# Kernel tuning notes

Measured on AMD Instinct MI355X. Metric: run time of the kernel, lower is better.

The kernel has to match this reference:

```python
import jax, jax.numpy as jnp
import numpy as np

B, N, D, H = 4, 2048, 256, 8
DH = D // H  # 32
EPS = 1e-5


def layernorm(x, g, b):
    mu = jnp.mean(x, axis=-1, keepdims=True)
    var = jnp.mean(jnp.square(x - mu), axis=-1, keepdims=True)
    return (x - mu) * jax.lax.rsqrt(var + EPS) * g + b


def setup_inputs() -> dict:
    key = jax.random.key(0)
    ks = jax.random.split(key, 16)
    s = 1.0 / np.sqrt(D)
    p = lambda k: jax.random.uniform(k, (D, D), jnp.float32, -s, s)
    return {
        "qdt": jax.random.normal(ks[0], (B, N, D), jnp.float32),
        "boxes": jax.random.normal(ks[1], (B, N, D), jnp.float32),
        "mask": jax.random.randint(ks[2], (N, N), 0, 2, jnp.int32),
        "Wq": p(ks[3]), "bq": jnp.zeros((D,), jnp.float32),
        "Wk": p(ks[4]), "bk": jnp.zeros((D,), jnp.float32),
        "Wv": p(ks[5]), "bv": jnp.zeros((D,), jnp.float32),
        "Wo": p(ks[6]), "bo": jnp.zeros((D,), jnp.float32),
        "W1": p(ks[7]), "b1": jnp.zeros((D,), jnp.float32),
        "W2": p(ks[8]), "b2": jnp.zeros((D,), jnp.float32),
        "g1": jnp.ones((D,), jnp.float32), "be1": jnp.zeros((D,), jnp.float32),
        "g2": jnp.ones((D,), jnp.float32), "be2": jnp.zeros((D,), jnp.float32),
    }


def reference(qdt, boxes, mask, Wq, bq, Wk, bk, Wv, bv, Wo, bo,
              W1, b1, W2, b2, g1, be1, g2, be2):
    # q = k = tgt = boxes + qdt  (dropout in eval mode -> identity)
    x = boxes + qdt  # [B,N,D]
    q = (x @ Wq + bq).reshape(B, N, H, DH)
    k = (x @ Wk + bk).reshape(B, N, H, DH)
    v = (x @ Wv + bv).reshape(B, N, H, DH)
    scores = jnp.einsum('bqhd,bkhd->bhqk', q, k) / np.sqrt(DH)
    # masked_fill(mask==0, -inf) then sigmoid  ==  sigmoid gated to 0 where masked
    attn = jnp.where(mask.astype(bool)[None, None, :, :],
                     jax.nn.sigmoid(scores), 0.0)
    o = jnp.einsum('bhqk,bkhd->bqhd', attn, v).reshape(B, N, D)
    attn_out = o @ Wo + bo
    tgt = layernorm(x + attn_out, g1, be1)
    ff = jax.nn.relu(tgt @ W1 + b1) @ W2 + b2
    tgt = layernorm(tgt + ff, g2, be2)
    return tgt
```

## Files before the change

### kernel.cpp

```cpp
#include <hip/hip_runtime.h>
#include <hip/hip_bf16.h>

typedef unsigned short u16;
typedef unsigned int u32;
typedef __attribute__((ext_vector_type(8))) short bf16x8;
typedef __attribute__((ext_vector_type(4))) float f32x4;

#define BB 4
#define NN 2048
#define DD 256
#define HH 8
#define LAMBDA (-0.2550351f)

__device__ inline u16 bfu(float f) {
  __hip_bfloat16 h = __float2bfloat16(f);
  return *reinterpret_cast<u16*>(&h);
}
__device__ inline bf16x8 asfrag(uint4 v) { return __builtin_bit_cast(bf16x8, v); }

__global__ __launch_bounds__(256) void prep_kernel(
    const float* __restrict__ qdt, const float* __restrict__ boxes,
    const int* __restrict__ mask,
    const float* __restrict__ Wq, const float* __restrict__ Wk, const float* __restrict__ Wv,
    const float* __restrict__ Wo, const float* __restrict__ W1, const float* __restrict__ W2,
    const float* __restrict__ bq, const float* __restrict__ bk, const float* __restrict__ bv,
    float* __restrict__ xp, u16* __restrict__ xb, unsigned char* __restrict__ m8,
    u16* __restrict__ wqkvT, u16* __restrict__ woT, u16* __restrict__ w1T, u16* __restrict__ w2T,
    float* __restrict__ bqkv) {
  const int bid = blockIdx.x, t = threadIdx.x;
  if (bid < 2048) {
    int i = bid * 256 + t;
    int row = i >> 6, q = i & 63;
    float4 a = ((const float4*)qdt)[i];
    float4 b = ((const float4*)boxes)[i];
    float4 v = make_float4(a.x + b.x, a.y + b.y, a.z + b.z, a.w + b.w);
    ((ushort4*)xb)[i] = make_ushort4(bfu(v.x), bfu(v.y), bfu(v.z), bfu(v.w));
    float* xr = xp + (size_t)row * 256;
    xr[((4*q+0) & 15) * 16 + ((4*q+0) >> 4)] = v.x;
    xr[((4*q+1) & 15) * 16 + ((4*q+1) >> 4)] = v.y;
    xr[((4*q+2) & 15) * 16 + ((4*q+2) >> 4)] = v.z;
    xr[((4*q+3) & 15) * 16 + ((4*q+3) >> 4)] = v.w;
  } else if (bid < 6144) {
    int i = (bid - 2048) * 256 + t;
    int4 m = ((const int4*)mask)[i];
    ((uchar4*)m8)[i] = make_uchar4((unsigned char)m.x, (unsigned char)m.y,
                                   (unsigned char)m.z, (unsigned char)m.w);
  } else {
    int i = (bid - 6144) * 256 + t;
    if (i < 196608) {
      int n = i >> 8, k = i & 255;
      const float* src = (n < 256) ? Wq : (n < 512 ? Wk : Wv);
      wqkvT[i] = bfu(src[k * 256 + (n & 255)]);
    } else if (i < 262144) {
      int j = i - 196608; int n = j >> 8, k = j & 255;
      woT[j] = bfu(Wo[k * 256 + n]);
    } else if (i < 327680) {
      int j = i - 262144; int n = j >> 8, k = j & 255;
      w1T[j] = bfu(W1[k * 256 + n]);
    } else if (i < 393216) {
      int j = i - 327680; int n = j >> 8, k = j & 255;
      w2T[j] = bfu(W2[k * 256 + n]);
    } else if (i < 393984) {
      int n = i - 393216;
      bqkv[n] = (n < 256) ? bq[n] : (n < 512 ? bk[n - 256] : bv[n - 512]);
    }
  }
}

__global__ __launch_bounds__(256) void gemm_qkvt_kernel(
    const u16* __restrict__ xb, const u16* __restrict__ wqkvT,
    const float* __restrict__ bqkv,
    u16* __restrict__ qout, u16* __restrict__ kout, u16* __restrict__ vtout) {
  __shared__ u16 At[64][264];
  __shared__ u16 Bs[64][264];
  const int bid = blockIdx.x;
  const bool isqk = bid < 1024;
  const u16* A  = isqk ? xb : (wqkvT + 512 * 256);
  const u16* Bt = isqk ? wqkvT : xb;
  const int m0 = isqk ? (bid >> 3) * 64 : ((bid - 1024) >> 7) * 64;
  const int n0 = isqk ? (bid & 7) * 64 : ((bid - 1024) & 127) * 64;
  const int t = threadIdx.x;
  {
    const int row = t >> 2, cb = (t & 3) * 64;
    const u16* ga = A  + (size_t)(m0 + row) * 256 + cb;
    const u16* gb = Bt + (size_t)(n0 + row) * 256 + cb;
#pragma unroll
    for (int i = 0; i < 8; ++i) {
      *(int4*)&At[row][cb + i * 8] = *(const int4*)(ga + i * 8);
      *(int4*)&Bs[row][cb + i * 8] = *(const int4*)(gb + i * 8);
    }
  }
  __syncthreads();
  const int w = t >> 6, l = t & 63, g = l >> 4, c = l & 15;
  f32x4 acc[4] = {};
#pragma unroll
  for (int kk = 0; kk < 256; kk += 32) {
    bf16x8 af = *(const bf16x8*)&At[w * 16 + c][kk + g * 8];
#pragma unroll
    for (int j = 0; j < 4; ++j) {
      bf16x8 bfr = *(const bf16x8*)&Bs[j * 16 + c][kk + g * 8];
      acc[j] = __builtin_amdgcn_mfma_f32_16x16x32_bf16(af, bfr, acc[j], 0, 0, 0);
    }
  }
  if (isqk) {
    if (n0 < 256) {
#pragma unroll
      for (int j = 0; j < 4; ++j)
#pragma unroll
        for (int r = 0; r < 4; ++r) {
          int m = m0 + w * 16 + g * 4 + r, n = n0 + j * 16 + c;
          qout[(size_t)m * 256 + n] = bfu((acc[j][r] + bqkv[n]) * LAMBDA);
        }
    } else {
#pragma unroll
      for (int j = 0; j < 4; ++j)
#pragma unroll
        for (int r = 0; r < 4; ++r) {
          int m = m0 + w * 16 + g * 4 + r, n = n0 + j * 16 + c;
          int ch = n - 256;
          kout[(size_t)((m >> 11) * 8 + (ch >> 5)) * 65536 + (size_t)(m & 2047) * 32 + (ch & 31)]
              = bfu(acc[j][r] + bqkv[n]);
        }
    }
  } else {
#pragma unroll
    for (int j = 0; j < 4; ++j)
#pragma unroll
      for (int r = 0; r < 4; ++r) {
        int m = m0 + w * 16 + g * 4 + r;
        int n = n0 + j * 16 + c;
        vtout[(size_t)m * 8192 + n] = bfu(acc[j][r] + bqkv[512 + m]);
      }
  }
}

__global__ __launch_bounds__(256) void attn_kernel(
    const u16* __restrict__ qb,
    const u16* __restrict__ kb,
    const u16* __restrict__ vtb,
    const unsigned char* __restrict__ m8,
    u16* __restrict__ ob) {
  __shared__ u32 Klds[2][64][20];
  __shared__ u32 Vlds[2][32][36];
  __shared__ unsigned char Mlds[2][64][64];
  __shared__ u32 Plds[4][16][36];

  const int bid = blockIdx.x;
  const int qt = bid & 31, h = (bid >> 5) & 7, b = bid >> 8;
  const int q0 = qt * 64;
  const int t = threadIdx.x, w = t >> 6, l = t & 63, g = l >> 4, c = l & 15;

  const bf16x8 qf = asfrag(*(const uint4*)(qb + (size_t)(b * NN + q0 + 16 * w + c) * 256 + h * 32 + 8 * g));
  f32x4 oacc[2] = {};

  const int srowK = t >> 2, ssegK = t & 3;
  const int srowV = t >> 3, ssegV = t & 7;
  const u16* kg = kb + (size_t)(b * 8 + h) * 65536 + srowK * 32 + ssegK * 8;
  const u16* vg = vtb + (size_t)(h * 32 + srowV) * 8192 + (size_t)b * NN + ssegV * 8;
  const unsigned char* mg = m8 + (size_t)(q0 + srowK) * NN + ssegK * 16;

  const int mb0 = (16 * ssegK + 8 * (srowK & 7)) & 63;
  const int mb1 = (mb0 + 8) & 63;

  uint4 krg = *(const uint4*)kg;
  uint4 vrg = *(const uint4*)vg;
  uint4 mrg = *(const uint4*)mg;
  *(uint4*)&Klds[0][srowK][ssegK * 4] = krg;
  *(uint4*)&Vlds[0][srowV][ssegV * 4] = vrg;
  *(uint2*)&Mlds[0][srowK][mb0] = make_uint2(mrg.x, mrg.y);
  *(uint2*)&Mlds[0][srowK][mb1] = make_uint2(mrg.z, mrg.w);
  __syncthreads();

  const f32x4 zf = {0.f, 0.f, 0.f, 0.f};
  u32* Pw = &Plds[w][0][0];

  for (int it = 0; it < 32; ++it) {
    const int cur = it & 1;
    if (it < 31) {
      const int kt = (it + 1) * 64;
      krg = *(const uint4*)(kg + (size_t)kt * 32);
      vrg = *(const uint4*)(vg + kt);
      mrg = *(const uint4*)(mg + kt);
    }
#pragma unroll
    for (int tt = 0; tt < 4; ++tt) {
      bf16x8 kf = asfrag(*(const uint4*)&Klds[cur][16 * tt + c][4 * g]);
      f32x4 s = __builtin_amdgcn_mfma_f32_16x16x32_bf16(kf, qf, zf, 0, 0, 0);
      u32 mdw = *(const u32*)&Mlds[cur][16 * w + c][(16 * tt + 4 * g + 8 * (c & 7)) & 63];
      float mf0 = (float)(mdw & 0xffu);
      float mf1 = (float)((mdw >> 8) & 0xffu);
      float mf2 = (float)((mdw >> 16) & 0xffu);
      float mf3 = (float)(mdw >> 24);
      float p0 = mf0 * __builtin_amdgcn_rcpf(1.f + __builtin_amdgcn_exp2f(s[0]));
      float p1 = mf1 * __builtin_amdgcn_rcpf(1.f + __builtin_amdgcn_exp2f(s[1]));
      float p2 = mf2 * __builtin_amdgcn_rcpf(1.f + __builtin_amdgcn_exp2f(s[2]));
      float p3 = mf3 * __builtin_amdgcn_rcpf(1.f + __builtin_amdgcn_exp2f(s[3]));
      u32 w0, w1;
      asm("v_cvt_pk_bf16_f32 %0, %1, %2" : "=v"(w0) : "v"(p0), "v"(p1));
      asm("v_cvt_pk_bf16_f32 %0, %1, %2" : "=v"(w1) : "v"(p2), "v"(p3));
      *(uint2*)&Pw[c * 36 + 8 * tt + 2 * g] = make_uint2(w0, w1);
    }
    asm volatile("s_waitcnt lgkmcnt(0)" ::: "memory");
    __builtin_amdgcn_sched_barrier(0);
#pragma unroll
    for (int kk = 0; kk < 2; ++kk) {
      bf16x8 pf = asfrag(*(const uint4*)&Pw[c * 36 + 16 * kk + 4 * g]);
#pragma unroll
      for (int d0 = 0; d0 < 2; ++d0) {
        bf16x8 vf = asfrag(*(const uint4*)&Vlds[cur][16 * d0 + c][16 * kk + 4 * g]);
        oacc[d0] = __builtin_amdgcn_mfma_f32_16x16x32_bf16(pf, vf, oacc[d0], 0, 0, 0);
      }
    }
    if (it < 31) {
      *(uint4*)&Klds[cur ^ 1][srowK][ssegK * 4] = krg;
      *(uint4*)&Vlds[cur ^ 1][srowV][ssegV * 4] = vrg;
      *(uint2*)&Mlds[cur ^ 1][srowK][mb0] = make_uint2(mrg.x, mrg.y);
      *(uint2*)&Mlds[cur ^ 1][srowK][mb1] = make_uint2(mrg.z, mrg.w);
    }
    __syncthreads();
  }

  const size_t obase = (size_t)(b * NN + q0 + 16 * w) * 256 + h * 32;
#pragma unroll
  for (int d0 = 0; d0 < 2; ++d0)
#pragma unroll
    for (int r = 0; r < 4; ++r)
      ob[obase + (size_t)(4 * g + r) * 256 + 16 * d0 + c] = bfu(oacc[d0][r]);
}

__global__ __launch_bounds__(256) void tail_kernel(
    const u16* __restrict__ obuf, const u16* __restrict__ woT,
    const u16* __restrict__ w1T, const u16* __restrict__ w2T,
    const float* __restrict__ xp,
    const float* __restrict__ bo, const float* __restrict__ b1, const float* __restrict__ b2,
    const float* __restrict__ g1, const float* __restrict__ be1,
    const float* __restrict__ g2, const float* __restrict__ be2,
    float* __restrict__ out) {
  __shared__ u16 A[16][264];
  __shared__ float T1[16][260];
  __shared__ float PS1[16][4], PS2[16][4];
  const int t = threadIdx.x, w = t >> 6, l = t & 63, g = l >> 4, c = l & 15;
  const int m0 = blockIdx.x * 16;
  const int n0 = w * 64;
  const f32x4 zf4 = {0.f, 0.f, 0.f, 0.f};

  {
    const int srow = t >> 4, sseg = t & 15;
#pragma unroll
    for (int i = 0; i < 2; ++i) {
      uint4 v = *(const uint4*)(obuf + (size_t)(m0 + srow) * 256 + (sseg + 16 * i) * 8);
      *(uint4*)&A[srow][(sseg + 16 * i) * 8] = v;
    }
  }
  __syncthreads();

  f32x4 acc[4];
  float mean[4], inv[4];

#pragma unroll
  for (int j = 0; j < 4; ++j) acc[j] = zf4;
#pragma unroll
  for (int kk = 0; kk < 256; kk += 32) {
    bf16x8 af = *(const bf16x8*)&A[c][kk + 8 * g];
#pragma unroll
    for (int j = 0; j < 4; ++j) {
      bf16x8 bfr = asfrag(*(const uint4*)(woT + (size_t)(n0 + 16 * j + c) * 256 + kk + 8 * g));
      acc[j] = __builtin_amdgcn_mfma_f32_16x16x32_bf16(af, bfr, acc[j], 0, 0, 0);
    }
  }
  {
    float bov[4];
#pragma unroll
    for (int j = 0; j < 4; ++j) bov[j] = bo[n0 + 16 * j + c];
#pragma unroll
    for (int r = 0; r < 4; ++r) {
      float4 xq = ((const float4*)(xp + (size_t)(m0 + 4 * g + r) * 256 + c * 16))[w];
      float xa[4] = {xq.x, xq.y, xq.z, xq.w};
      float a1 = 0.f, a2 = 0.f;
#pragma unroll
      for (int j = 0; j < 4; ++j) {
        float z = acc[j][r] + bov[j] + xa[j];
        T1[4 * g + r][n0 + 16 * j + c] = z;
        a1 += z; a2 += z * z;
      }
#pragma unroll
      for (int off = 1; off < 16; off <<= 1) {
        a1 += __shfl_xor(a1, off);
        a2 += __shfl_xor(a2, off);
      }
      if (c == 0) { PS1[4 * g + r][w] = a1; PS2[4 * g + r][w] = a2; }
    }
  }
  __syncthreads();
#pragma unroll
  for (int r = 0; r < 4; ++r) {
    const int row = 4 * g + r;
    float s1 = PS1[row][0] + PS1[row][1] + PS1[row][2] + PS1[row][3];
    float s2 = PS2[row][0] + PS2[row][1] + PS2[row][2] + PS2[row][3];
    mean[r] = s1 * (1.f / 256.f);
    inv[r] = rsqrtf(s2 * (1.f / 256.f) - mean[r] * mean[r] + 1e-5f);
  }
#pragma unroll
  for (int j = 0; j < 4; ++j) {
    const int n = n0 + 16 * j + c;
    const float gv = g1[n], bev = be1[n];
#pragma unroll
    for (int r = 0; r < 4; ++r) {
      float v = (T1[4 * g + r][n] - mean[r]) * inv[r] * gv + bev;
      T1[4 * g + r][n] = v;
      A[4 * g + r][n] = bfu(v);
    }
  }
  __syncthreads();

#pragma unroll
  for (int j = 0; j < 4; ++j) acc[j] = zf4;
#pragma unroll
  for (int kk = 0; kk < 256; kk += 32) {
    bf16x8 af = *(const bf16x8*)&A[c][kk + 8 * g];
#pragma unroll
    for (int j = 0; j < 4; ++j) {
      bf16x8 bfr = asfrag(*(const uint4*)(w1T + (size_t)(n0 + 16 * j + c) * 256 + kk + 8 * g));
      acc[j] = __builtin_amdgcn_mfma_f32_16x16x32_bf16(af, bfr, acc[j], 0, 0, 0);
    }
  }
  __syncthreads();
#pragma unroll
  for (int j = 0; j < 4; ++j) {
    const int n = n0 + 16 * j + c;
    const float bv = b1[n];
#pragma unroll
    for (int r = 0; r < 4; ++r) {
      float v = acc[j][r] + bv;
      A[4 * g + r][n] = bfu(v > 0.f ? v : 0.f);
    }
  }
  __syncthreads();

#pragma unroll
  for (int j = 0; j < 4; ++j) acc[j] = zf4;
#pragma unroll
  for (int kk = 0; kk < 256; kk += 32) {
    bf16x8 af = *(const bf16x8*)&A[c][kk + 8 * g];
#pragma unroll
    for (int j = 0; j < 4; ++j) {
      bf16x8 bfr = asfrag(*(const uint4*)(w2T + (size_t)(n0 + 16 * j + c) * 256 + kk + 8 * g));
      acc[j] = __builtin_amdgcn_mfma_f32_16x16x32_bf16(af, bfr, acc[j], 0, 0, 0);
    }
  }
  {
    float b2v[4];
#pragma unroll
    for (int j = 0; j < 4; ++j) b2v[j] = b2[n0 + 16 * j + c];
#pragma unroll
    for (int r = 0; r < 4; ++r) {
      float a1 = 0.f, a2 = 0.f;
#pragma unroll
      for (int j = 0; j < 4; ++j) {
        const int n = n0 + 16 * j + c;
        float z = acc[j][r] + b2v[j] + T1[4 * g + r][n];
        T1[4 * g + r][n] = z;
        a1 += z; a2 += z * z;
      }
#pragma unroll
      for (int off = 1; off < 16; off <<= 1) {
        a1 += __shfl_xor(a1, off);
        a2 += __shfl_xor(a2, off);
      }
      if (c == 0) { PS1[4 * g + r][w] = a1; PS2[4 * g + r][w] = a2; }
    }
  }
  __syncthreads();
#pragma unroll
  for (int r = 0; r < 4; ++r) {
    const int row = 4 * g + r;
    float s1 = PS1[row][0] + PS1[row][1] + PS1[row][2] + PS1[row][3];
    float s2 = PS2[row][0] + PS2[row][1] + PS2[row][2] + PS2[row][3];
    mean[r] = s1 * (1.f / 256.f);
    inv[r] = rsqrtf(s2 * (1.f / 256.f) - mean[r] * mean[r] + 1e-5f);
  }
#pragma unroll
  for (int j = 0; j < 4; ++j) {
    const int n = n0 + 16 * j + c;
    const float gv = g2[n], bev = be2[n];
#pragma unroll
    for (int r = 0; r < 4; ++r)
      out[(size_t)(m0 + 4 * g + r) * 256 + n] = (T1[4 * g + r][n] - mean[r]) * inv[r] * gv + bev;
  }
}

extern "C" void kernel_launch(void* const* d_in, const int* in_sizes, int n_in,
                              void* d_out, int out_size, void* d_ws, size_t ws_size,
                              hipStream_t stream) {
  const float* qdt   = (const float*)d_in[0];
  const float* boxes = (const float*)d_in[1];
  const int*   mask  = (const int*)d_in[2];
  const float* Wq = (const float*)d_in[3];
  const float* bq = (const float*)d_in[4];
  const float* Wk = (const float*)d_in[5];
  const float* bk = (const float*)d_in[6];
  const float* Wv = (const float*)d_in[7];
  const float* bv = (const float*)d_in[8];
  const float* Wo = (const float*)d_in[9];
  const float* bo = (const float*)d_in[10];
  const float* W1 = (const float*)d_in[11];
  const float* b1 = (const float*)d_in[12];
  const float* W2 = (const float*)d_in[13];
  const float* b2 = (const float*)d_in[14];
  const float* g1  = (const float*)d_in[15];
  const float* be1 = (const float*)d_in[16];
  const float* g2  = (const float*)d_in[17];
  const float* be2 = (const float*)d_in[18];

  char* ws = (char*)d_ws;
  float* xp    = (float*)(ws + 0);
  u16*   xb    = (u16*)  (ws + 8388608);
  u16*   qbuf  = (u16*)  (ws + 12582912);
  u16*   kbuf  = (u16*)  (ws + 16777216);
  u16*   vtbuf = (u16*)  (ws + 20971520);
  u16*   obuf  = (u16*)  (ws + 25165824);
  u16*   wqkvT = (u16*)  (ws + 46137344);
  u16*   woT   = (u16*)  (ws + 46530560);
  u16*   w1T   = (u16*)  (ws + 46661632);
  u16*   w2T   = (u16*)  (ws + 46792704);
  float* bqkv  = (float*)(ws + 46923776);
  unsigned char* m8 = (unsigned char*)(ws + 46926848);

  prep_kernel<<<7683, 256, 0, stream>>>(qdt, boxes, mask, Wq, Wk, Wv, Wo, W1, W2,
                                        bq, bk, bv, xp, xb, m8,
                                        wqkvT, woT, w1T, w2T, bqkv);
  gemm_qkvt_kernel<<<1536, 256, 0, stream>>>(xb, wqkvT, bqkv, qbuf, kbuf, vtbuf);
  attn_kernel<<<1024, 256, 0, stream>>>(qbuf, kbuf, vtbuf, m8, obuf);
  tail_kernel<<<512, 256, 0, stream>>>(obuf, woT, w1T, w2T, xp,
                                       bo, b1, b2, g1, be1, g2, be2, (float*)d_out);
}
```

Before: 112.9 us.

## Process 32 rows per tail block and keep residual in registers

```diff
diff --git a/kernel.cpp b/kernel.cpp
--- a/kernel.cpp
+++ b/kernel.cpp
@@ -236,36 +236,39 @@
     const float* __restrict__ g1, const float* __restrict__ be1,
     const float* __restrict__ g2, const float* __restrict__ be2,
     float* __restrict__ out) {
-  __shared__ u16 A[16][264];
-  __shared__ float T1[16][260];
-  __shared__ float PS1[16][4], PS2[16][4];
+  __shared__ u16 A[32][264];
+  __shared__ float PS1[32][4], PS2[32][4];
   const int t = threadIdx.x, w = t >> 6, l = t & 63, g = l >> 4, c = l & 15;
-  const int m0 = blockIdx.x * 16;
+  const int m0 = blockIdx.x * 32;
   const int n0 = w * 64;
   const f32x4 zf4 = {0.f, 0.f, 0.f, 0.f};
 
   {
-    const int srow = t >> 4, sseg = t & 15;
-#pragma unroll
-    for (int i = 0; i < 2; ++i) {
-      uint4 v = *(const uint4*)(obuf + (size_t)(m0 + srow) * 256 + (sseg + 16 * i) * 8);
-      *(uint4*)&A[srow][(sseg + 16 * i) * 8] = v;
-    }
-  }
-  __syncthreads();
-
-  f32x4 acc[4];
-  float mean[4], inv[4];
-
-#pragma unroll
-  for (int j = 0; j < 4; ++j) acc[j] = zf4;
+    const int srow = t >> 3, sseg = t & 7;
+#pragma unroll
+    for (int i = 0; i < 4; ++i) {
+      uint4 v = *(const uint4*)(obuf + (size_t)(m0 + srow) * 256 + (sseg + 8 * i) * 8);
+      *(uint4*)&A[srow][(sseg + 8 * i) * 8] = v;
+    }
+  }
+  __syncthreads();
+
+  f32x4 acc[2][4], t1[2][4];
+  float mean[2][4], inv[2][4];
+
+#pragma unroll
+  for (int rg = 0; rg < 2; ++rg)
+#pragma unroll
+    for (int j = 0; j < 4; ++j) acc[rg][j] = zf4;
 #pragma unroll
   for (int kk = 0; kk < 256; kk += 32) {
-    bf16x8 af = *(const bf16x8*)&A[c][kk + 8 * g];
+    bf16x8 af0 = *(const bf16x8*)&A[c][kk + 8 * g];
+    bf16x8 af1 = *(const bf16x8*)&A[16 + c][kk + 8 * g];
 #pragma unroll
     for (int j = 0; j < 4; ++j) {
       bf16x8 bfr = asfrag(*(const uint4*)(woT + (size_t)(n0 + 16 * j + c) * 256 + kk + 8 * g));
-      acc[j] = __builtin_amdgcn_mfma_f32_16x16x32_bf16(af, bfr, acc[j], 0, 0, 0);
+      acc[0][j] = __builtin_amdgcn_mfma_f32_16x16x32_bf16(af0, bfr, acc[0][j], 0, 0, 0);
+      acc[1][j] = __builtin_amdgcn_mfma_f32_16x16x32_bf16(af1, bfr, acc[1][j], 0, 0, 0);
     }
   }
   {
@@ -273,55 +276,66 @@
 #pragma unroll
     for (int j = 0; j < 4; ++j) bov[j] = bo[n0 + 16 * j + c];
 #pragma unroll
+    for (int rg = 0; rg < 2; ++rg)
+#pragma unroll
+      for (int r = 0; r < 4; ++r) {
+        const int rl = 16 * rg + 4 * g + r;
+        float4 xq = ((const float4*)(xp + (size_t)(m0 + rl) * 256 + c * 16))[w];
+        float xa[4] = {xq.x, xq.y, xq.z, xq.w};
+        float a1 = 0.f, a2 = 0.f;
+#pragma unroll
+        for (int j = 0; j < 4; ++j) {
+          float z = acc[rg][j][r] + bov[j] + xa[j];
+          t1[rg][j][r] = z;
+          a1 += z; a2 += z * z;
+        }
+#pragma unroll
+        for (int off = 1; off < 16; off <<= 1) {
+          a1 += __shfl_xor(a1, off);
+          a2 += __shfl_xor(a2, off);
+        }
+        if (c == 0) { PS1[rl][w] = a1; PS2[rl][w] = a2; }
+      }
+  }
+  __syncthreads();
+#pragma unroll
+  for (int rg = 0; rg < 2; ++rg)
+#pragma unroll
     for (int r = 0; r < 4; ++r) {
-      float4 xq = ((const float4*)(xp + (size_t)(m0 + 4 * g + r) * 256 + c * 16))[w];
-      float xa[4] = {xq.x, xq.y, xq.z, xq.w};
-      float a1 = 0.f, a2 = 0.f;
-#pragma unroll
-      for (int j = 0; j < 4; ++j) {
-        float z = acc[j][r] + bov[j] + xa[j];
-        T1[4 * g + r][n0 + 16 * j + c] = z;
-        a1 += z; a2 += z * z;
-      }
-#pragma unroll
-      for (int off = 1; off < 16; off <<= 1) {
-        a1 += __shfl_xor(a1, off);
-        a2 += __shfl_xor(a2, off);
-      }
-      if (c == 0) { PS1[4 * g + r][w] = a1; PS2[4 * g + r][w] = a2; }
-    }
-  }
-  __syncthreads();
-#pragma unroll
-  for (int r = 0; r < 4; ++r) {
-    const int row = 4 * g + r;
-    float s1 = PS1[row][0] + PS1[row][1] + PS1[row][2] + PS1[row][3];
-    float s2 = PS2[row][0] + PS2[row][1] + PS2[row][2] + PS2[row][3];
-    mean[r] = s1 * (1.f / 256.f);
-    inv[r] = rsqrtf(s2 * (1.f / 256.f) - mean[r] * mean[r] + 1e-5f);
-  }
+      const int rl = 16 * rg + 4 * g + r;
+      float s1 = PS1[rl][0] + PS1[rl][1] + PS1[rl][2] + PS1[rl][3];
+      float s2 = PS2[rl][0] + PS2[rl][1] + PS2[rl][2] + PS2[rl][3];
+      mean[rg][r] = s1 * (1.f / 256.f);
+      inv[rg][r] = rsqrtf(s2 * (1.f / 256.f) - mean[rg][r] * mean[rg][r] + 1e-5f);
+    }
 #pragma unroll
   for (int j = 0; j < 4; ++j) {
     const int n = n0 + 16 * j + c;
     const float gv = g1[n], bev = be1[n];
 #pragma unroll
-    for (int r = 0; r < 4; ++r) {
-      float v = (T1[4 * g + r][n] - mean[r]) * inv[r] * gv + bev;
-      T1[4 * g + r][n] = v;
-      A[4 * g + r][n] = bfu(v);
-    }
-  }
-  __syncthreads();
-
-#pragma unroll
-  for (int j = 0; j < 4; ++j) acc[j] = zf4;
+    for (int rg = 0; rg < 2; ++rg)
+#pragma unroll
+      for (int r = 0; r < 4; ++r) {
+        float v = (t1[rg][j][r] - mean[rg][r]) * inv[rg][r] * gv + bev;
+        t1[rg][j][r] = v;
+        A[16 * rg + 4 * g + r][n] = bfu(v);
+      }
+  }
+  __syncthreads();
+
+#pragma unroll
+  for (int rg = 0; rg < 2; ++rg)
+#pragma unroll
+    for (int j = 0; j < 4; ++j) acc[rg][j] = zf4;
 #pragma unroll
   for (int kk = 0; kk < 256; kk += 32) {
-    bf16x8 af = *(const bf16x8*)&A[c][kk + 8 * g];
+    bf16x8 af0 = *(const bf16x8*)&A[c][kk + 8 * g];
+    bf16x8 af1 = *(const bf16x8*)&A[16 + c][kk + 8 * g];
 #pragma unroll
     for (int j = 0; j < 4; ++j) {
       bf16x8 bfr = asfrag(*(const uint4*)(w1T + (size_t)(n0 + 16 * j + c) * 256 + kk + 8 * g));
-      acc[j] = __builtin_amdgcn_mfma_f32_16x16x32_bf16(af, bfr, acc[j], 0, 0, 0);
+      acc[0][j] = __builtin_amdgcn_mfma_f32_16x16x32_bf16(af0, bfr, acc[0][j], 0, 0, 0);
+      acc[1][j] = __builtin_amdgcn_mfma_f32_16x16x32_bf16(af1, bfr, acc[1][j], 0, 0, 0);
     }
   }
   __syncthreads();
@@ -330,22 +344,28 @@
     const int n = n0 + 16 * j + c;
     const float bv = b1[n];
 #pragma unroll
-    for (int r = 0; r < 4; ++r) {
-      float v = acc[j][r] + bv;
-      A[4 * g + r][n] = bfu(v > 0.f ? v : 0.f);
-    }
-  }
-  __syncthreads();
-
-#pragma unroll
-  for (int j = 0; j < 4; ++j) acc[j] = zf4;
+    for (int rg = 0; rg < 2; ++rg)
+#pragma unroll
+      for (int r = 0; r < 4; ++r) {
+        float v = acc[rg][j][r] + bv;
+        A[16 * rg + 4 * g + r][n] = bfu(v > 0.f ? v : 0.f);
+      }
+  }
+  __syncthreads();
+
+#pragma unroll
+  for (int rg = 0; rg < 2; ++rg)
+#pragma unroll
+    for (int j = 0; j < 4; ++j) acc[rg][j] = zf4;
 #pragma unroll
   for (int kk = 0; kk < 256; kk += 32) {
-    bf16x8 af = *(const bf16x8*)&A[c][kk + 8 * g];
+    bf16x8 af0 = *(const bf16x8*)&A[c][kk + 8 * g];
+    bf16x8 af1 = *(const bf16x8*)&A[16 + c][kk + 8 * g];
 #pragma unroll
     for (int j = 0; j < 4; ++j) {
       bf16x8 bfr = asfrag(*(const uint4*)(w2T + (size_t)(n0 + 16 * j + c) * 256 + kk + 8 * g));
-      acc[j] = __builtin_amdgcn_mfma_f32_16x16x32_bf16(af, bfr, acc[j], 0, 0, 0);
+      acc[0][j] = __builtin_amdgcn_mfma_f32_16x16x32_bf16(af0, bfr, acc[0][j], 0, 0, 0);
+      acc[1][j] = __builtin_amdgcn_mfma_f32_16x16x32_bf16(af1, bfr, acc[1][j], 0, 0, 0);
     }
   }
   {
@@ -353,39 +373,46 @@
 #pragma unroll
     for (int j = 0; j < 4; ++j) b2v[j] = b2[n0 + 16 * j + c];
 #pragma unroll
+    for (int rg = 0; rg < 2; ++rg)
+#pragma unroll
+      for (int r = 0; r < 4; ++r) {
+        const int rl = 16 * rg + 4 * g + r;
+        float a1 = 0.f, a2 = 0.f;
+#pragma unroll
+        for (int j = 0; j < 4; ++j) {
+          float z = acc[rg][j][r] + b2v[j] + t1[rg][j][r];
+          t1[rg][j][r] = z;
+          a1 += z; a2 += z * z;
+        }
+#pragma unroll
+        for (int off = 1; off < 16; off <<= 1) {
+          a1 += __shfl_xor(a1, off);
+          a2 += __shfl_xor(a2, off);
+        }
+        if (c == 0) { PS1[rl][w] = a1; PS2[rl][w] = a2; }
+      }
+  }
+  __syncthreads();
+#pragma unroll
+  for (int rg = 0; rg < 2; ++rg)
+#pragma unroll
     for (int r = 0; r < 4; ++r) {
-      float a1 = 0.f, a2 = 0.f;
-#pragma unroll
-      for (int j = 0; j < 4; ++j) {
-        const int n = n0 + 16 * j + c;
-        float z = acc[j][r] + b2v[j] + T1[4 * g + r][n];
-        T1[4 * g + r][n] = z;
-        a1 += z; a2 += z * z;
-      }
-#pragma unroll
-      for (int off = 1; off < 16; off <<= 1) {
-        a1 += __shfl_xor(a1, off);
-        a2 += __shfl_xor(a2, off);
-      }
-      if (c == 0) { PS1[4 * g + r][w] = a1; PS2[4 * g + r][w] = a2; }
-    }
-  }
-  __syncthreads();
-#pragma unroll
-  for (int r = 0; r < 4; ++r) {
-    const int row = 4 * g + r;
-    float s1 = PS1[row][0] + PS1[row][1] + PS1[row][2] + PS1[row][3];
-    float s2 = PS2[row][0] + PS2[row][1] + PS2[row][2] + PS2[row][3];
-    mean[r] = s1 * (1.f / 256.f);
-    inv[r] = rsqrtf(s2 * (1.f / 256.f) - mean[r] * mean[r] + 1e-5f);
-  }
+      const int rl = 16 * rg + 4 * g + r;
+      float s1 = PS1[rl][0] + PS1[rl][1] + PS1[rl][2] + PS1[rl][3];
+      float s2 = PS2[rl][0] + PS2[rl][1] + PS2[rl][2] + PS2[rl][3];
+      mean[rg][r] = s1 * (1.f / 256.f);
+      inv[rg][r] = rsqrtf(s2 * (1.f / 256.f) - mean[rg][r] * mean[rg][r] + 1e-5f);
+    }
 #pragma unroll
   for (int j = 0; j < 4; ++j) {
     const int n = n0 + 16 * j + c;
     const float gv = g2[n], bev = be2[n];
 #pragma unroll
-    for (int r = 0; r < 4; ++r)
-      out[(size_t)(m0 + 4 * g + r) * 256 + n] = (T1[4 * g + r][n] - mean[r]) * inv[r] * gv + bev;
+    for (int rg = 0; rg < 2; ++rg)
+#pragma unroll
+      for (int r = 0; r < 4; ++r)
+        out[(size_t)(m0 + 16 * rg + 4 * g + r) * 256 + n]
+            = (t1[rg][j][r] - mean[rg][r]) * inv[rg][r] * gv + bev;
   }
 }
 
@@ -431,6 +458,6 @@
                                         wqkvT, woT, w1T, w2T, bqkv);
   gemm_qkvt_kernel<<<1536, 256, 0, stream>>>(xb, wqkvT, bqkv, qbuf, kbuf, vtbuf);
   attn_kernel<<<1024, 256, 0, stream>>>(qbuf, kbuf, vtbuf, m8, obuf);
-  tail_kernel<<<512, 256, 0, stream>>>(obuf, woT, w1T, w2T, xp,
+  tail_kernel<<<256, 256, 0, stream>>>(obuf, woT, w1T, w2T, xp,
                                        bo, b1, b2, g1, be1, g2, be2, (float*)d_out);
 }
```

Result: no change. 112.3 us (-0.6%).
